# Kernel optimization log

Measured on AMD Instinct MI355X. Metric: run time of the kernel, lower is better.

## Reference

```python
import jax, jax.numpy as jnp
import numpy as np

N_PARTICLES = 100000
STATE_DIM = 64          # 3 + 2*2 + 57
MSG_OUT = 64
HIDDEN = 32
N_EDGES = 1600000


def _init_linear(key, fan_in, fan_out):
    kw, kb = jax.random.split(key)
    bound = 1.0 / np.sqrt(fan_in)
    W = jax.random.uniform(kw, (fan_in, fan_out), minval=-bound, maxval=bound, dtype=jnp.float32)
    b = jax.random.uniform(kb, (fan_out,), minval=-bound, maxval=bound, dtype=jnp.float32)
    return W, b


def setup_inputs() -> dict:
    key = jax.random.key(0)
    ks = jax.random.split(key, 8)
    x = jax.random.normal(ks[0], (N_PARTICLES, STATE_DIM), dtype=jnp.float32)
    edge_index = jax.random.randint(ks[1], (2, N_EDGES), 0, N_PARTICLES, dtype=jnp.int64)
    # message conv MLP: [2*STATE_DIM] -> 32 -> 32 -> MSG_OUT
    mW1, mb1 = _init_linear(ks[2], 2 * STATE_DIM, HIDDEN)
    mW2, mb2 = _init_linear(ks[3], HIDDEN, HIDDEN)
    mW3, mb3 = _init_linear(ks[4], HIDDEN, MSG_OUT)
    # own_state_nn MLP: [STATE_DIM + MSG_OUT] -> 32 -> 32 -> STATE_DIM
    oW1, ob1 = _init_linear(ks[5], STATE_DIM + MSG_OUT, HIDDEN)
    oW2, ob2 = _init_linear(ks[6], HIDDEN, HIDDEN)
    oW3, ob3 = _init_linear(ks[7], HIDDEN, STATE_DIM)
    return {"x": x, "edge_index": edge_index,
            "mW1": mW1, "mb1": mb1, "mW2": mW2, "mb2": mb2, "mW3": mW3, "mb3": mb3,
            "oW1": oW1, "ob1": ob1, "oW2": oW2, "ob2": ob2, "oW3": oW3, "ob3": ob3}


def _mlp3(h, W1, b1, W2, b2, W3, b3):
    h = jax.nn.relu(h @ W1 + b1)
    h = jax.nn.relu(h @ W2 + b2)
    return h @ W3 + b3


def reference(x, edge_index, mW1, mb1, mW2, mb2, mW3, mb3,
              oW1, ob1, oW2, ob2, oW3, ob3):
    src, dst = edge_index[0], edge_index[1]
    # edge-wise message: MLP over [x_src || x_dst]  -> [E, MSG_OUT]
    e_feat = jnp.concatenate([x[src], x[dst]], axis=-1)  # [E, 2*STATE_DIM]
    m = _mlp3(e_feat, mW1, mb1, mW2, mb2, mW3, mb3)
    # scatter-sum aggregation at destination node
    messages = jax.ops.segment_sum(m, dst, num_segments=x.shape[0])  # [N, MSG_OUT]
    combined = jnp.concatenate([x, messages], axis=-1)  # [N, STATE_DIM+MSG_OUT]
    new_state = _mlp3(combined, oW1, ob1, oW2, ob2, oW3, ob3)
    return new_state
```

## Files before the change

### kernel.cpp

```cpp
#include <hip/hip_runtime.h>

#define NP 100000
#define NE 1600000
#define SD 64
#define HID 32
#define MSG 64
#define NP_PAD 100352
#define NTILE (NP / 16)
#define TILE_BLOCKS ((NTILE + 3) / 4)
#define BINSZ 512
#define NBIN ((NP + BINSZ - 1) / BINSZ)
#define EPW 8192
#define NWG ((NE + EPW - 1) / EPW)

typedef float v4f __attribute__((ext_vector_type(4)));
typedef short v4s __attribute__((ext_vector_type(4)));
typedef short v8s __attribute__((ext_vector_type(8)));
typedef __bf16 v8bf __attribute__((ext_vector_type(8)));

#define WQ_FRAGS 56

__device__ __forceinline__ v4f MFMA32(v8s a, v8s b, v4f c) {
  return __builtin_amdgcn_mfma_f32_16x16x32_bf16(
      __builtin_bit_cast(v8bf, a), __builtin_bit_cast(v8bf, b), c, 0, 0, 0);
}

__device__ __forceinline__ short f2bf(float f) {
  return __builtin_bit_cast(short, (__bf16)f);
}
__device__ __forceinline__ float bf2f(short s) {
  unsigned u = ((unsigned)(unsigned short)s) << 16;
  return __builtin_bit_cast(float, u);
}

__device__ __forceinline__ v4f mfma3(v8s ah, v8s al, v8s bh, v8s bl, v4f c) {
  c = MFMA32(al, bh, c);
  c = MFMA32(ah, bl, c);
  c = MFMA32(ah, bh, c);
  return c;
}

__device__ __forceinline__ void load_wfrag(const float* __restrict__ W, int ld,
                                           int kb, int m0, int lq, int l15,
                                           v8s* hi, v8s* lo) {
  v8s h, l;
#pragma unroll
  for (int j = 0; j < 8; ++j) {
    int k = kb + ((j < 4) ? (4 * lq + j) : (16 + 4 * lq + (j - 4)));
    float v = W[k * ld + m0 + l15];
    short hb = f2bf(v);
    h[j] = hb;
    l[j] = f2bf(v - bf2f(hb));
  }
  *hi = h;
  *lo = l;
}

__device__ __forceinline__ void split8(v4f a, v4f b, v8s* hi, v8s* lo) {
  v8s h, l;
#pragma unroll
  for (int j = 0; j < 4; ++j) {
    short ha = f2bf(a[j]); h[j] = ha; l[j] = f2bf(a[j] - bf2f(ha));
    short hb = f2bf(b[j]); h[j + 4] = hb; l[j + 4] = f2bf(b[j] - bf2f(hb));
  }
  *hi = h;
  *lo = l;
}

__device__ __forceinline__ void load_xfrag(const float* xs, int kb, int lq,
                                           v8s* hi, v8s* lo) {
  v4f a = *reinterpret_cast<const v4f*>(xs + kb + 4 * lq);
  v4f b = *reinterpret_cast<const v4f*>(xs + kb + 16 + 4 * lq);
  split8(a, b, hi, lo);
}

__device__ __forceinline__ void chain_frag(v4f d0, v4f d1, v8s* hi, v8s* lo) {
  v4f a, b;
#pragma unroll
  for (int j = 0; j < 4; ++j) {
    a[j] = fmaxf(d0[j], 0.f);
    b[j] = fmaxf(d1[j], 0.f);
  }
  split8(a, b, hi, lo);
}

__device__ __forceinline__ v8s chain_hi(v4f d0, v4f d1) {
  v8s h;
#pragma unroll
  for (int j = 0; j < 4; ++j) {
    h[j] = f2bf(fmaxf(d0[j], 0.f));
    h[j + 4] = f2bf(fmaxf(d1[j], 0.f));
  }
  return h;
}

__global__ __launch_bounds__(256, 2) void setup_kernel(
    const float* __restrict__ x, const int* __restrict__ ei,
    const float* __restrict__ mW1, const float* __restrict__ mb1,
    const float* __restrict__ mW2, const float* __restrict__ mW3,
    const float* __restrict__ oW1, const float* __restrict__ oW2,
    const float* __restrict__ oW3,
    int* __restrict__ gOff, short* __restrict__ wqs,
    float* __restrict__ h1d_buf, short* __restrict__ h1s_buf) {
  __shared__ int cnt[NBIN];
  const int blk = blockIdx.x;

  if (blk < NWG) {
    for (int i = threadIdx.x; i < NBIN; i += 256) cnt[i] = 0;
    __syncthreads();
    const int e0 = blk * EPW;
    const int e1 = (e0 + EPW < NE) ? e0 + EPW : NE;
    for (int e = e0 + threadIdx.x; e < e1; e += 256)
      atomicAdd(&cnt[ei[NE + e] >> 9], 1);
    __syncthreads();
    for (int i = threadIdx.x; i < NBIN; i += 256) gOff[i * NWG + blk] = cnt[i];
    return;
  }

  const int lane = threadIdx.x & 63;
  const int l15 = lane & 15;
  const int lq = lane >> 4;

  if (blk == NWG) {
    if (threadIdx.x >= 64) return;
    v8s* wq = reinterpret_cast<v8s*>(wqs);
    v8s h, l;
#pragma unroll
    for (int t = 0; t < 2; ++t)
#pragma unroll
      for (int kc = 0; kc < 2; ++kc) {
        load_wfrag(mW1, HID, kc * 32, t * 16, lq, l15, &h, &l);
        wq[(t * 2 + kc) * 64 + lane] = h;
        wq[(4 + t * 2 + kc) * 64 + lane] = l;
        load_wfrag(mW1, HID, 64 + kc * 32, t * 16, lq, l15, &h, &l);
        wq[(8 + t * 2 + kc) * 64 + lane] = h;
        wq[(12 + t * 2 + kc) * 64 + lane] = l;
      }
#pragma unroll
    for (int t = 0; t < 2; ++t) {
      load_wfrag(mW2, HID, 0, t * 16, lq, l15, &h, &l);
      wq[(16 + t) * 64 + lane] = h;
      wq[(18 + t) * 64 + lane] = l;
    }
#pragma unroll
    for (int t = 0; t < 4; ++t) {
      load_wfrag(mW3, MSG, 0, t * 16, lq, l15, &h, &l);
      wq[(20 + t) * 64 + lane] = h;
      wq[(24 + t) * 64 + lane] = l;
    }
#pragma unroll
    for (int t = 0; t < 2; ++t)
#pragma unroll
      for (int kc = 0; kc < 4; ++kc) {
        load_wfrag(oW1, HID, kc * 32, t * 16, lq, l15, &h, &l);
        wq[(28 + t * 4 + kc) * 64 + lane] = h;
        wq[(36 + t * 4 + kc) * 64 + lane] = l;
      }
#pragma unroll
    for (int t = 0; t < 2; ++t) {
      load_wfrag(oW2, HID, 0, t * 16, lq, l15, &h, &l);
      wq[(44 + t) * 64 + lane] = h;
      wq[(46 + t) * 64 + lane] = l;
    }
#pragma unroll
    for (int t = 0; t < 4; ++t) {
      load_wfrag(oW3, SD, 0, t * 16, lq, l15, &h, &l);
      wq[(48 + t) * 64 + lane] = h;
      wq[(52 + t) * 64 + lane] = l;
    }
    return;
  }

  const int tile = ((blk - NWG - 1) * 256 + (int)threadIdx.x) >> 6;
  if (tile >= NTILE) return;
  const int node = tile * 16 + l15;

  v4f d0, d1, s0 = {0.f, 0.f, 0.f, 0.f}, s1 = {0.f, 0.f, 0.f, 0.f};
#pragma unroll
  for (int q = 0; q < 4; ++q) {
    d0[q] = mb1[4 * lq + q];
    d1[q] = mb1[16 + 4 * lq + q];
  }
#pragma unroll
  for (int kc = 0; kc < 2; ++kc) {
    v8s xh, xl, wh, wl;
    load_xfrag(x + (size_t)node * SD, kc * 32, lq, &xh, &xl);
    load_wfrag(mW1, HID, 64 + kc * 32, 0, lq, l15, &wh, &wl);
    d0 = mfma3(wh, wl, xh, xl, d0);
    load_wfrag(mW1, HID, 64 + kc * 32, 16, lq, l15, &wh, &wl);
    d1 = mfma3(wh, wl, xh, xl, d1);
    load_wfrag(mW1, HID, kc * 32, 0, lq, l15, &wh, &wl);
    s0 = mfma3(wh, wl, xh, xl, s0);
    load_wfrag(mW1, HID, kc * 32, 16, lq, l15, &wh, &wl);
    s1 = mfma3(wh, wl, xh, xl, s1);
  }
  *reinterpret_cast<v4f*>(h1d_buf + (size_t)node * HID + 4 * lq) = d0;
  *reinterpret_cast<v4f*>(h1d_buf + (size_t)node * HID + 16 + 4 * lq) = d1;
  v4s q0, q1;
#pragma unroll
  for (int q = 0; q < 4; ++q) {
    q0[q] = f2bf(s0[q]);
    q1[q] = f2bf(s1[q]);
  }
  *reinterpret_cast<v4s*>(h1s_buf + (size_t)node * HID + 4 * lq) = q0;
  *reinterpret_cast<v4s*>(h1s_buf + (size_t)node * HID + 16 + 4 * lq) = q1;
}


__global__ __launch_bounds__(256) void scan_bins_kernel(
    int* __restrict__ gOff, int* __restrict__ binStart) {
  __shared__ int sh[256];
  const int b = threadIdx.x;
  int run = 0;
  if (b < NBIN) {
    int4* row = reinterpret_cast<int4*>(gOff + b * NWG);
#pragma unroll 4
    for (int i = 0; i < NWG / 4; ++i) {
      int4 v = row[i];
      int4 w;
      w.x = run; run += v.x;
      w.y = run; run += v.y;
      w.z = run; run += v.z;
      w.w = run; run += v.w;
      row[i] = w;
    }
  }
  sh[b] = run;
  __syncthreads();
  for (int off = 1; off < 256; off <<= 1) {
    int a = (b >= off) ? sh[b - off] : 0;
    __syncthreads();
    sh[b] += a;
    __syncthreads();
  }
  const int excl = sh[b] - run;
  if (b <= NBIN) binStart[b] = excl;
  if (b < NBIN) {
    int4* row = reinterpret_cast<int4*>(gOff + b * NWG);
#pragma unroll 4
    for (int i = 0; i < NWG / 4; ++i) {
      int4 v = row[i];
      v.x += excl; v.y += excl; v.z += excl; v.w += excl;
      row[i] = v;
    }
  }
}

__global__ __launch_bounds__(256) void bin_scatter_kernel(
    const int* __restrict__ ei, const int* __restrict__ gOff,
    unsigned* __restrict__ pairs) {
  __shared__ int cur[NBIN];
  const int w = blockIdx.x;
  for (int i = threadIdx.x; i < NBIN; i += 256) cur[i] = gOff[i * NWG + w];
  __syncthreads();
  const int e0 = w * EPW;
  const int e1 = (e0 + EPW < NE) ? e0 + EPW : NE;
  for (int e = e0 + threadIdx.x; e < e1; e += 256) {
    unsigned s = (unsigned)ei[e];
    unsigned d = (unsigned)ei[NE + e];
    int pos = atomicAdd(&cur[d >> 9], 1);
    pairs[pos] = (s << 9) | (d & (BINSZ - 1));
  }
}

__global__ __launch_bounds__(512) void bin_csr_kernel(
    const unsigned* __restrict__ pairs, const int* __restrict__ binStart,
    int2* __restrict__ co, int* __restrict__ csr_src) {
  __shared__ int sh[BINSZ];
  __shared__ int cu[BINSZ];
  const int b = blockIdx.x;
  const int t = threadIdx.x;
  cu[t] = 0;
  __syncthreads();
  const int p0 = binStart[b], p1 = binStart[b + 1];
  for (int p = p0 + t; p < p1; p += BINSZ)
    atomicAdd(&cu[pairs[p] & (BINSZ - 1)], 1);
  __syncthreads();
  const int v = cu[t];
  sh[t] = v;
  __syncthreads();
  for (int off = 1; off < BINSZ; off <<= 1) {
    int a = (t >= off) ? sh[t - off] : 0;
    __syncthreads();
    sh[t] += a;
    __syncthreads();
  }
  const int excl = sh[t] - v;
  const int node = b * BINSZ + t;
  if (node < NP) co[node] = make_int2(p0 + excl, v);
  cu[t] = excl;
  __syncthreads();
  for (int p = p0 + t; p < p1; p += BINSZ) {
    unsigned pr = pairs[p];
    int loc = atomicAdd(&cu[pr & (BINSZ - 1)], 1);
    csr_src[p0 + loc] = (int)(pr >> 9);
  }
}

__global__ __launch_bounds__(256, 4) void edge_mfma_kernel(
    const short* __restrict__ h1s, const float* __restrict__ h1d_buf,
    const short* __restrict__ wqs, const int2* __restrict__ co,
    const int* __restrict__ csr_src, const float* __restrict__ mb2,
    float* __restrict__ rsum) {
  const int lane = threadIdx.x & 63;
  const int l15 = lane & 15;
  const int lq = lane >> 4;
  const int wid = (blockIdx.x * 256 + threadIdx.x) >> 6;
  const int nw = gridDim.x * 4;
  const v8s* wq = reinterpret_cast<const v8s*>(wqs);

  const v8s w2h0 = wq[16 * 64 + lane], w2h1 = wq[17 * 64 + lane];
  const v8s w2l0 = wq[18 * 64 + lane], w2l1 = wq[19 * 64 + lane];
  v4f bb0, bb1;
#pragma unroll
  for (int q = 0; q < 4; ++q) {
    bb0[q] = mb2[4 * lq + q];
    bb1[q] = mb2[16 + 4 * lq + q];
  }

  for (int n = wid; n < NP; n += nw) {
    const int2 c = co[n];
    const int off = c.x, cnt = c.y;
    const int ng = (cnt + 15) >> 4;

    const v4f h1d0 = *reinterpret_cast<const v4f*>(h1d_buf + (size_t)n * HID + 4 * lq);
    const v4f h1d1 = *reinterpret_cast<const v4f*>(h1d_buf + (size_t)n * HID + 16 + 4 * lq);

    v4f r0 = {0.f, 0.f, 0.f, 0.f}, r1 = {0.f, 0.f, 0.f, 0.f};

    int sa = (l15 < cnt) ? csr_src[off + l15] : 0;
    v4s a0 = *reinterpret_cast<const v4s*>(h1s + (size_t)sa * HID + 4 * lq);
    v4s b0 = *reinterpret_cast<const v4s*>(h1s + (size_t)sa * HID + 16 + 4 * lq);
    int sb = (l15 < cnt - 16) ? csr_src[off + 16 + l15] : 0;
    v4s a1 = *reinterpret_cast<const v4s*>(h1s + (size_t)sb * HID + 4 * lq);
    v4s b1 = *reinterpret_cast<const v4s*>(h1s + (size_t)sb * HID + 16 + 4 * lq);

    int rem = cnt;
    for (int g = 0; g < ng; ++g) {
      int sc = (l15 < rem - 32) ? csr_src[off + (g + 2) * 16 + l15] : 0;

      v4f d0, d1;
#pragma unroll
      for (int q = 0; q < 4; ++q) {
        d0[q] = h1d0[q] + bf2f(a0[q]);
        d1[q] = h1d1[q] + bf2f(b0[q]);
      }

      v8s ph = chain_hi(d0, d1);
      v4f e0 = bb0, e1 = bb1;
      e0 = MFMA32(w2h0, ph, e0);
      e0 = MFMA32(w2l0, ph, e0);
      e1 = MFMA32(w2h1, ph, e1);
      e1 = MFMA32(w2l1, ph, e1);

      if (l15 < rem) {
#pragma unroll
        for (int j = 0; j < 4; ++j) {
          r0[j] += fmaxf(e0[j], 0.f);
          r1[j] += fmaxf(e1[j], 0.f);
        }
      }

      v4s a2 = *reinterpret_cast<const v4s*>(h1s + (size_t)sc * HID + 4 * lq);
      v4s b2 = *reinterpret_cast<const v4s*>(h1s + (size_t)sc * HID + 16 + 4 * lq);

      a0 = a1; b0 = b1;
      a1 = a2; b1 = b2;
      rem -= 16;
    }

#pragma unroll
    for (int j = 0; j < 4; ++j) {
      float a = r0[j], b = r1[j];
      a += __shfl_xor(a, 1); a += __shfl_xor(a, 2);
      a += __shfl_xor(a, 4); a += __shfl_xor(a, 8);
      b += __shfl_xor(b, 1); b += __shfl_xor(b, 2);
      b += __shfl_xor(b, 4); b += __shfl_xor(b, 8);
      r0[j] = a; r1[j] = b;
    }
    if (l15 == 0) {
      *reinterpret_cast<v4f*>(rsum + (size_t)n * HID + 4 * lq) = r0;
      *reinterpret_cast<v4f*>(rsum + (size_t)n * HID + 16 + 4 * lq) = r1;
    }
  }
}

__global__ __launch_bounds__(256, 2) void fused_tail_kernel(
    const float* __restrict__ x, const short* __restrict__ wqs,
    const float* __restrict__ rsum, const int2* __restrict__ co,
    const float* __restrict__ mb3,
    const float* __restrict__ ob1, const float* __restrict__ ob2,
    const float* __restrict__ ob3,
    float* __restrict__ out) {
  const int lane = threadIdx.x & 63;
  const int l15 = lane & 15;
  const int lq = lane >> 4;
  const int tile = (blockIdx.x * 256 + threadIdx.x) >> 6;
  if (tile >= NTILE) return;
  const v8s* wq = reinterpret_cast<const v8s*>(wqs);

  const int node = tile * 16 + l15;
  const float fc = (float)co[node].y;

  v4f ra = *reinterpret_cast<const v4f*>(rsum + (size_t)node * HID + 4 * lq);
  v4f rb = *reinterpret_cast<const v4f*>(rsum + (size_t)node * HID + 16 + 4 * lq);
  v8s bh, bl;
  split8(ra, rb, &bh, &bl);

  v4f m[4];
#pragma unroll
  for (int t = 0; t < 4; ++t) {
    v4f c = {0.f, 0.f, 0.f, 0.f};
    c = mfma3(wq[(20 + t) * 64 + lane], wq[(24 + t) * 64 + lane], bh, bl, c);
#pragma unroll
    for (int q = 0; q < 4; ++q) c[q] += fc * mb3[t * 16 + 4 * lq + q];
    m[t] = c;
  }

  v4f d0, d1;
#pragma unroll
  for (int q = 0; q < 4; ++q) {
    d0[q] = ob1[4 * lq + q];
    d1[q] = ob1[16 + 4 * lq + q];
  }
#pragma unroll
  for (int kc = 0; kc < 2; ++kc) {
    v8s xh, xl;
    load_xfrag(x + (size_t)node * SD, kc * 32, lq, &xh, &xl);
    d0 = mfma3(wq[(28 + kc) * 64 + lane], wq[(36 + kc) * 64 + lane], xh, xl, d0);
    d1 = mfma3(wq[(32 + kc) * 64 + lane], wq[(40 + kc) * 64 + lane], xh, xl, d1);
  }
#pragma unroll
  for (int kc = 0; kc < 2; ++kc) {
    v8s mh, ml;
    split8(m[kc * 2], m[kc * 2 + 1], &mh, &ml);
    d0 = mfma3(wq[(30 + kc) * 64 + lane], wq[(38 + kc) * 64 + lane], mh, ml, d0);
    d1 = mfma3(wq[(34 + kc) * 64 + lane], wq[(42 + kc) * 64 + lane], mh, ml, d1);
  }

  v8s ph, pl;
  chain_frag(d0, d1, &ph, &pl);
  v4f e0, e1;
#pragma unroll
  for (int q = 0; q < 4; ++q) {
    e0[q] = ob2[4 * lq + q];
    e1[q] = ob2[16 + 4 * lq + q];
  }
  e0 = mfma3(wq[44 * 64 + lane], wq[46 * 64 + lane], ph, pl, e0);
  e1 = mfma3(wq[45 * 64 + lane], wq[47 * 64 + lane], ph, pl, e1);

  v8s rh, rl;
  chain_frag(e0, e1, &rh, &rl);
  float* orow = out + (size_t)node * SD;
#pragma unroll
  for (int t = 0; t < 4; ++t) {
    v4f c;
#pragma unroll
    for (int q = 0; q < 4; ++q) c[q] = ob3[t * 16 + 4 * lq + q];
    c = mfma3(wq[(48 + t) * 64 + lane], wq[(52 + t) * 64 + lane], rh, rl, c);
    *reinterpret_cast<v4f*>(orow + t * 16 + 4 * lq) = c;
  }
}

extern "C" void kernel_launch(void* const* d_in, const int* in_sizes, int n_in,
                              void* d_out, int out_size, void* d_ws,
                              size_t ws_size, hipStream_t stream) {
  const float* x = (const float*)d_in[0];
  const int* ei = (const int*)d_in[1];
  const float* mW1 = (const float*)d_in[2];
  const float* mb1 = (const float*)d_in[3];
  const float* mW2 = (const float*)d_in[4];
  const float* mb2 = (const float*)d_in[5];
  const float* mW3 = (const float*)d_in[6];
  const float* mb3 = (const float*)d_in[7];
  const float* oW1 = (const float*)d_in[8];
  const float* ob1 = (const float*)d_in[9];
  const float* oW2 = (const float*)d_in[10];
  const float* ob2 = (const float*)d_in[11];
  const float* oW3 = (const float*)d_in[12];
  const float* ob3 = (const float*)d_in[13];
  float* out = (float*)d_out;

  float* h1d_buf = (float*)d_out;
  short* h1s_buf = (short*)((char*)d_out + (size_t)NP * HID * 4);

  char* p = (char*)d_ws;
  short* wqs = (short*)p;            p += (size_t)WQ_FRAGS * 64 * 16;
  int* gOff = (int*)p;               p += (size_t)NBIN * NWG * 4;
  int* binStart = (int*)p;           p += 200 * 4;
  int2* co = (int2*)p;               p += (size_t)NP_PAD * 8;
  int* csr_src = (int*)p;            p += (size_t)NE * 4;
  unsigned* pairs = (unsigned*)p;
  float* rsum = (float*)p;

  setup_kernel<<<NWG + 1 + TILE_BLOCKS, 256, 0, stream>>>(
      x, ei, mW1, mb1, mW2, mW3, oW1, oW2, oW3, gOff, wqs, h1d_buf, h1s_buf);

  scan_bins_kernel<<<1, 256, 0, stream>>>(gOff, binStart);
  bin_scatter_kernel<<<NWG, 256, 0, stream>>>(ei, gOff, pairs);
  bin_csr_kernel<<<NBIN, 512, 0, stream>>>(pairs, binStart, co, csr_src);

  edge_mfma_kernel<<<2048, 256, 0, stream>>>(
      h1s_buf, h1d_buf, wqs, co, csr_src, mb2, rsum);

  fused_tail_kernel<<<TILE_BLOCKS, 256, 0, stream>>>(
      x, wqs, rsum, co, mb3, ob1, ob2, ob3, out);
}
```

Baseline: 158.8 us.

## Process two destination nodes per wave with interleaved gather pipelines

The per-node edge aggregation kernel now has each wave handle two consecutive destination nodes at once, interleaving their 16-edge groups. The goal is more independent gathers and MFMA chains in flight per wave, hiding gather latency. The prefetch depth per node drops from two groups to one, and the shorter node idles while the longer one finishes, so the wave does divergent, partly wasted iterations. NP is even, so pairing the nodes is safe.

```diff
diff --git a/kernel.cpp b/kernel.cpp
--- a/kernel.cpp
+++ b/kernel.cpp
@@ -318,69 +318,104 @@
     bb1[q] = mb2[16 + 4 * lq + q];
   }
 
-  for (int n = wid; n < NP; n += nw) {
-    const int2 c = co[n];
-    const int off = c.x, cnt = c.y;
-    const int ng = (cnt + 15) >> 4;
-
-    const v4f h1d0 = *reinterpret_cast<const v4f*>(h1d_buf + (size_t)n * HID + 4 * lq);
-    const v4f h1d1 = *reinterpret_cast<const v4f*>(h1d_buf + (size_t)n * HID + 16 + 4 * lq);
-
-    v4f r0 = {0.f, 0.f, 0.f, 0.f}, r1 = {0.f, 0.f, 0.f, 0.f};
-
-    int sa = (l15 < cnt) ? csr_src[off + l15] : 0;
-    v4s a0 = *reinterpret_cast<const v4s*>(h1s + (size_t)sa * HID + 4 * lq);
-    v4s b0 = *reinterpret_cast<const v4s*>(h1s + (size_t)sa * HID + 16 + 4 * lq);
-    int sb = (l15 < cnt - 16) ? csr_src[off + 16 + l15] : 0;
-    v4s a1 = *reinterpret_cast<const v4s*>(h1s + (size_t)sb * HID + 4 * lq);
-    v4s b1 = *reinterpret_cast<const v4s*>(h1s + (size_t)sb * HID + 16 + 4 * lq);
-
-    int rem = cnt;
-    for (int g = 0; g < ng; ++g) {
-      int sc = (l15 < rem - 32) ? csr_src[off + (g + 2) * 16 + l15] : 0;
-
-      v4f d0, d1;
-#pragma unroll
-      for (int q = 0; q < 4; ++q) {
-        d0[q] = h1d0[q] + bf2f(a0[q]);
-        d1[q] = h1d1[q] + bf2f(b0[q]);
-      }
-
-      v8s ph = chain_hi(d0, d1);
-      v4f e0 = bb0, e1 = bb1;
-      e0 = MFMA32(w2h0, ph, e0);
-      e0 = MFMA32(w2l0, ph, e0);
-      e1 = MFMA32(w2h1, ph, e1);
-      e1 = MFMA32(w2l1, ph, e1);
-
-      if (l15 < rem) {
-#pragma unroll
-        for (int j = 0; j < 4; ++j) {
-          r0[j] += fmaxf(e0[j], 0.f);
-          r1[j] += fmaxf(e1[j], 0.f);
+  for (int n = wid * 2; n < NP; n += 2 * nw) {
+    const int4 cc = *reinterpret_cast<const int4*>(co + n);
+    const int offA = cc.x, cntA = cc.y;
+    const int offB = cc.z, cntB = cc.w;
+    const int ngA = (cntA + 15) >> 4;
+    const int ngB = (cntB + 15) >> 4;
+    const int ngM = ngA > ngB ? ngA : ngB;
+
+    const v4f hA0 = *reinterpret_cast<const v4f*>(h1d_buf + (size_t)n * HID + 4 * lq);
+    const v4f hA1 = *reinterpret_cast<const v4f*>(h1d_buf + (size_t)n * HID + 16 + 4 * lq);
+    const v4f hB0 = *reinterpret_cast<const v4f*>(h1d_buf + (size_t)(n + 1) * HID + 4 * lq);
+    const v4f hB1 = *reinterpret_cast<const v4f*>(h1d_buf + (size_t)(n + 1) * HID + 16 + 4 * lq);
+
+    v4f rA0 = {0.f, 0.f, 0.f, 0.f}, rA1 = {0.f, 0.f, 0.f, 0.f};
+    v4f rB0 = {0.f, 0.f, 0.f, 0.f}, rB1 = {0.f, 0.f, 0.f, 0.f};
+
+    int sA = (l15 < cntA) ? csr_src[offA + l15] : 0;
+    int sB = (l15 < cntB) ? csr_src[offB + l15] : 0;
+    v4s aA = *reinterpret_cast<const v4s*>(h1s + (size_t)sA * HID + 4 * lq);
+    v4s bA = *reinterpret_cast<const v4s*>(h1s + (size_t)sA * HID + 16 + 4 * lq);
+    v4s aB = *reinterpret_cast<const v4s*>(h1s + (size_t)sB * HID + 4 * lq);
+    v4s bB = *reinterpret_cast<const v4s*>(h1s + (size_t)sB * HID + 16 + 4 * lq);
+
+    int remA = cntA, remB = cntB;
+    for (int g = 0; g < ngM; ++g) {
+      int sAn = (l15 < remA - 16) ? csr_src[offA + (g + 1) * 16 + l15] : 0;
+      int sBn = (l15 < remB - 16) ? csr_src[offB + (g + 1) * 16 + l15] : 0;
+
+      if (g < ngA) {
+        v4f d0, d1;
+#pragma unroll
+        for (int q = 0; q < 4; ++q) {
+          d0[q] = hA0[q] + bf2f(aA[q]);
+          d1[q] = hA1[q] + bf2f(bA[q]);
+        }
+        v8s ph = chain_hi(d0, d1);
+        v4f e0 = bb0, e1 = bb1;
+        e0 = MFMA32(w2h0, ph, e0);
+        e0 = MFMA32(w2l0, ph, e0);
+        e1 = MFMA32(w2h1, ph, e1);
+        e1 = MFMA32(w2l1, ph, e1);
+        if (l15 < remA) {
+#pragma unroll
+          for (int j = 0; j < 4; ++j) {
+            rA0[j] += fmaxf(e0[j], 0.f);
+            rA1[j] += fmaxf(e1[j], 0.f);
+          }
         }
       }
-
-      v4s a2 = *reinterpret_cast<const v4s*>(h1s + (size_t)sc * HID + 4 * lq);
-      v4s b2 = *reinterpret_cast<const v4s*>(h1s + (size_t)sc * HID + 16 + 4 * lq);
-
-      a0 = a1; b0 = b1;
-      a1 = a2; b1 = b2;
-      rem -= 16;
+      aA = *reinterpret_cast<const v4s*>(h1s + (size_t)sAn * HID + 4 * lq);
+      bA = *reinterpret_cast<const v4s*>(h1s + (size_t)sAn * HID + 16 + 4 * lq);
+
+      if (g < ngB) {
+        v4f d0, d1;
+#pragma unroll
+        for (int q = 0; q < 4; ++q) {
+          d0[q] = hB0[q] + bf2f(aB[q]);
+          d1[q] = hB1[q] + bf2f(bB[q]);
+        }
+        v8s ph = chain_hi(d0, d1);
+        v4f e0 = bb0, e1 = bb1;
+        e0 = MFMA32(w2h0, ph, e0);
+        e0 = MFMA32(w2l0, ph, e0);
+        e1 = MFMA32(w2h1, ph, e1);
+        e1 = MFMA32(w2l1, ph, e1);
+        if (l15 < remB) {
+#pragma unroll
+          for (int j = 0; j < 4; ++j) {
+            rB0[j] += fmaxf(e0[j], 0.f);
+            rB1[j] += fmaxf(e1[j], 0.f);
+          }
+        }
+      }
+      aB = *reinterpret_cast<const v4s*>(h1s + (size_t)sBn * HID + 4 * lq);
+      bB = *reinterpret_cast<const v4s*>(h1s + (size_t)sBn * HID + 16 + 4 * lq);
+
+      remA -= 16;
+      remB -= 16;
     }
 
 #pragma unroll
     for (int j = 0; j < 4; ++j) {
-      float a = r0[j], b = r1[j];
+      float a = rA0[j], b = rA1[j], c = rB0[j], d = rB1[j];
       a += __shfl_xor(a, 1); a += __shfl_xor(a, 2);
       a += __shfl_xor(a, 4); a += __shfl_xor(a, 8);
       b += __shfl_xor(b, 1); b += __shfl_xor(b, 2);
       b += __shfl_xor(b, 4); b += __shfl_xor(b, 8);
-      r0[j] = a; r1[j] = b;
+      c += __shfl_xor(c, 1); c += __shfl_xor(c, 2);
+      c += __shfl_xor(c, 4); c += __shfl_xor(c, 8);
+      d += __shfl_xor(d, 1); d += __shfl_xor(d, 2);
+      d += __shfl_xor(d, 4); d += __shfl_xor(d, 8);
+      rA0[j] = a; rA1[j] = b; rB0[j] = c; rB1[j] = d;
     }
     if (l15 == 0) {
-      *reinterpret_cast<v4f*>(rsum + (size_t)n * HID + 4 * lq) = r0;
-      *reinterpret_cast<v4f*>(rsum + (size_t)n * HID + 16 + 4 * lq) = r1;
+      *reinterpret_cast<v4f*>(rsum + (size_t)n * HID + 4 * lq) = rA0;
+      *reinterpret_cast<v4f*>(rsum + (size_t)n * HID + 16 + 4 * lq) = rA1;
+      *reinterpret_cast<v4f*>(rsum + (size_t)(n + 1) * HID + 4 * lq) = rB0;
+      *reinterpret_cast<v4f*>(rsum + (size_t)(n + 1) * HID + 16 + 4 * lq) = rB1;
     }
   }
 }
```

Result: faster. 154.9 us (median of 3 runs) (-2.4%).

## Drop per-node CSR build; aggregate edge messages per bin with LDS atomics

Applied to the files above, without the earlier changes.

Removes the bin_csr kernel and the per-node CSR walk. A new bin_edge kernel reads the binned (src, local dst) pairs directly, runs the edge MLP with MFMA and accumulates ReLU outputs into a padded LDS tile using float atomics, along with per-node edge counts. Bins shrink to 256 nodes and each bin is split across two blocks that write separate partial sums; the tail kernel adds the two partials. This saves a kernel launch and a full pass over the edge list, but adds many LDS atomics, larger intermediate buffers, and a floating-point summation order that is no longer fixed.

```diff
diff --git a/kernel.cpp b/kernel.cpp
--- a/kernel.cpp
+++ b/kernel.cpp
@@ -8,8 +8,9 @@
 #define NP_PAD 100352
 #define NTILE (NP / 16)
 #define TILE_BLOCKS ((NTILE + 3) / 4)
-#define BINSZ 512
+#define BINSZ 256
 #define NBIN ((NP + BINSZ - 1) / BINSZ)
+#define RPITCH 33
 #define EPW 8192
 #define NWG ((NE + EPW - 1) / EPW)
 
@@ -111,7 +112,7 @@
     const int e0 = blk * EPW;
     const int e1 = (e0 + EPW < NE) ? e0 + EPW : NE;
     for (int e = e0 + threadIdx.x; e < e1; e += 256)
-      atomicAdd(&cnt[ei[NE + e] >> 9], 1);
+      atomicAdd(&cnt[ei[NE + e] >> 8], 1);
     __syncthreads();
     for (int i = threadIdx.x; i < NBIN; i += 256) gOff[i * NWG + blk] = cnt[i];
     return;
@@ -207,9 +208,9 @@
 }
 
 
-__global__ __launch_bounds__(256) void scan_bins_kernel(
+__global__ __launch_bounds__(512) void scan_bins_kernel(
     int* __restrict__ gOff, int* __restrict__ binStart) {
-  __shared__ int sh[256];
+  __shared__ int sh[512];
   const int b = threadIdx.x;
   int run = 0;
   if (b < NBIN) {
@@ -227,7 +228,7 @@
   }
   sh[b] = run;
   __syncthreads();
-  for (int off = 1; off < 256; off <<= 1) {
+  for (int off = 1; off < 512; off <<= 1) {
     int a = (b >= off) ? sh[b - off] : 0;
     __syncthreads();
     sh[b] += a;
@@ -258,57 +259,31 @@
   for (int e = e0 + threadIdx.x; e < e1; e += 256) {
     unsigned s = (unsigned)ei[e];
     unsigned d = (unsigned)ei[NE + e];
-    int pos = atomicAdd(&cur[d >> 9], 1);
-    pairs[pos] = (s << 9) | (d & (BINSZ - 1));
-  }
-}
-
-__global__ __launch_bounds__(512) void bin_csr_kernel(
-    const unsigned* __restrict__ pairs, const int* __restrict__ binStart,
-    int2* __restrict__ co, int* __restrict__ csr_src) {
-  __shared__ int sh[BINSZ];
-  __shared__ int cu[BINSZ];
-  const int b = blockIdx.x;
-  const int t = threadIdx.x;
-  cu[t] = 0;
-  __syncthreads();
-  const int p0 = binStart[b], p1 = binStart[b + 1];
-  for (int p = p0 + t; p < p1; p += BINSZ)
-    atomicAdd(&cu[pairs[p] & (BINSZ - 1)], 1);
-  __syncthreads();
-  const int v = cu[t];
-  sh[t] = v;
-  __syncthreads();
-  for (int off = 1; off < BINSZ; off <<= 1) {
-    int a = (t >= off) ? sh[t - off] : 0;
-    __syncthreads();
-    sh[t] += a;
-    __syncthreads();
-  }
-  const int excl = sh[t] - v;
-  const int node = b * BINSZ + t;
-  if (node < NP) co[node] = make_int2(p0 + excl, v);
-  cu[t] = excl;
-  __syncthreads();
-  for (int p = p0 + t; p < p1; p += BINSZ) {
-    unsigned pr = pairs[p];
-    int loc = atomicAdd(&cu[pr & (BINSZ - 1)], 1);
-    csr_src[p0 + loc] = (int)(pr >> 9);
-  }
-}
-
-__global__ __launch_bounds__(256, 4) void edge_mfma_kernel(
+    int pos = atomicAdd(&cur[d >> 8], 1);
+    pairs[pos] = (s << 8) | (d & (BINSZ - 1));
+  }
+}
+
+__global__ __launch_bounds__(512, 4) void bin_edge_kernel(
     const short* __restrict__ h1s, const float* __restrict__ h1d_buf,
-    const short* __restrict__ wqs, const int2* __restrict__ co,
-    const int* __restrict__ csr_src, const float* __restrict__ mb2,
-    float* __restrict__ rsum) {
-  const int lane = threadIdx.x & 63;
+    const short* __restrict__ wqs, const unsigned* __restrict__ pairs,
+    const int* __restrict__ binStart, const float* __restrict__ mb2,
+    float* __restrict__ rsumP, int* __restrict__ cntP) {
+  __shared__ float r_lds[BINSZ * RPITCH];
+  __shared__ int cnt_lds[BINSZ];
+  const int tid = threadIdx.x;
+  const int lane = tid & 63;
   const int l15 = lane & 15;
   const int lq = lane >> 4;
-  const int wid = (blockIdx.x * 256 + threadIdx.x) >> 6;
-  const int nw = gridDim.x * 4;
+  const int wv = tid >> 6;
+  const int b = blockIdx.x >> 1;
+  const int half = blockIdx.x & 1;
+
+  for (int i = tid; i < BINSZ * RPITCH; i += 512) r_lds[i] = 0.f;
+  for (int i = tid; i < BINSZ; i += 512) cnt_lds[i] = 0;
+  __syncthreads();
+
   const v8s* wq = reinterpret_cast<const v8s*>(wqs);
-
   const v8s w2h0 = wq[16 * 64 + lane], w2h1 = wq[17 * 64 + lane];
   const v8s w2l0 = wq[18 * 64 + lane], w2l1 = wq[19 * 64 + lane];
   v4f bb0, bb1;
@@ -318,76 +293,81 @@
     bb1[q] = mb2[16 + 4 * lq + q];
   }
 
-  for (int n = wid; n < NP; n += nw) {
-    const int2 c = co[n];
-    const int off = c.x, cnt = c.y;
-    const int ng = (cnt + 15) >> 4;
-
-    const v4f h1d0 = *reinterpret_cast<const v4f*>(h1d_buf + (size_t)n * HID + 4 * lq);
-    const v4f h1d1 = *reinterpret_cast<const v4f*>(h1d_buf + (size_t)n * HID + 16 + 4 * lq);
-
-    v4f r0 = {0.f, 0.f, 0.f, 0.f}, r1 = {0.f, 0.f, 0.f, 0.f};
-
-    int sa = (l15 < cnt) ? csr_src[off + l15] : 0;
-    v4s a0 = *reinterpret_cast<const v4s*>(h1s + (size_t)sa * HID + 4 * lq);
-    v4s b0 = *reinterpret_cast<const v4s*>(h1s + (size_t)sa * HID + 16 + 4 * lq);
-    int sb = (l15 < cnt - 16) ? csr_src[off + 16 + l15] : 0;
-    v4s a1 = *reinterpret_cast<const v4s*>(h1s + (size_t)sb * HID + 4 * lq);
-    v4s b1 = *reinterpret_cast<const v4s*>(h1s + (size_t)sb * HID + 16 + 4 * lq);
-
-    int rem = cnt;
-    for (int g = 0; g < ng; ++g) {
-      int sc = (l15 < rem - 32) ? csr_src[off + (g + 2) * 16 + l15] : 0;
-
-      v4f d0, d1;
+  const int p0 = binStart[b], p1 = binStart[b + 1];
+  const int mid = p0 + ((p1 - p0 + 1) >> 1);
+  const int q0 = half ? mid : p0;
+  const int q1 = half ? p1 : mid;
+  const int nodeBase = b * BINSZ;
+
+  int p = q0 + wv * 16;
+  unsigned pr = (p + l15 < q1) ? pairs[p + l15] : 0u;
+  int dl = (int)(pr & (BINSZ - 1));
+  {
+    int src = (int)(pr >> 8);
+  }
+  int src0 = (int)(pr >> 8);
+  v4s a = *reinterpret_cast<const v4s*>(h1s + (size_t)src0 * HID + 4 * lq);
+  v4s c = *reinterpret_cast<const v4s*>(h1s + (size_t)src0 * HID + 16 + 4 * lq);
+  const float* hd = h1d_buf + (size_t)(nodeBase + dl) * HID;
+  v4f hd0 = *reinterpret_cast<const v4f*>(hd + 4 * lq);
+  v4f hd1 = *reinterpret_cast<const v4f*>(hd + 16 + 4 * lq);
+
+  for (; p < q1; p += 128) {
+    const int pn = p + 128 + l15;
+    unsigned prn = (pn < q1) ? pairs[pn] : 0u;
+    int srcn = (int)(prn >> 8);
+    int dln = (int)(prn & (BINSZ - 1));
+    v4s an = *reinterpret_cast<const v4s*>(h1s + (size_t)srcn * HID + 4 * lq);
+    v4s cn = *reinterpret_cast<const v4s*>(h1s + (size_t)srcn * HID + 16 + 4 * lq);
+    const float* hdn = h1d_buf + (size_t)(nodeBase + dln) * HID;
+    v4f hdn0 = *reinterpret_cast<const v4f*>(hdn + 4 * lq);
+    v4f hdn1 = *reinterpret_cast<const v4f*>(hdn + 16 + 4 * lq);
+
+    v4f d0, d1;
+#pragma unroll
+    for (int q = 0; q < 4; ++q) {
+      d0[q] = hd0[q] + bf2f(a[q]);
+      d1[q] = hd1[q] + bf2f(c[q]);
+    }
+    v8s ph = chain_hi(d0, d1);
+    v4f e0 = bb0, e1 = bb1;
+    e0 = MFMA32(w2h0, ph, e0);
+    e0 = MFMA32(w2l0, ph, e0);
+    e1 = MFMA32(w2h1, ph, e1);
+    e1 = MFMA32(w2l1, ph, e1);
+
+    if (p + l15 < q1) {
+      float* rr = r_lds + dl * RPITCH;
 #pragma unroll
       for (int q = 0; q < 4; ++q) {
-        d0[q] = h1d0[q] + bf2f(a0[q]);
-        d1[q] = h1d1[q] + bf2f(b0[q]);
+        atomicAdd(&rr[4 * lq + q], fmaxf(e0[q], 0.f));
+        atomicAdd(&rr[16 + 4 * lq + q], fmaxf(e1[q], 0.f));
       }
-
-      v8s ph = chain_hi(d0, d1);
-      v4f e0 = bb0, e1 = bb1;
-      e0 = MFMA32(w2h0, ph, e0);
-      e0 = MFMA32(w2l0, ph, e0);
-      e1 = MFMA32(w2h1, ph, e1);
-      e1 = MFMA32(w2l1, ph, e1);
-
-      if (l15 < rem) {
-#pragma unroll
-        for (int j = 0; j < 4; ++j) {
-          r0[j] += fmaxf(e0[j], 0.f);
-          r1[j] += fmaxf(e1[j], 0.f);
-        }
-      }
-
-      v4s a2 = *reinterpret_cast<const v4s*>(h1s + (size_t)sc * HID + 4 * lq);
-      v4s b2 = *reinterpret_cast<const v4s*>(h1s + (size_t)sc * HID + 16 + 4 * lq);
-
-      a0 = a1; b0 = b1;
-      a1 = a2; b1 = b2;
-      rem -= 16;
-    }
-
-#pragma unroll
-    for (int j = 0; j < 4; ++j) {
-      float a = r0[j], b = r1[j];
-      a += __shfl_xor(a, 1); a += __shfl_xor(a, 2);
-      a += __shfl_xor(a, 4); a += __shfl_xor(a, 8);
-      b += __shfl_xor(b, 1); b += __shfl_xor(b, 2);
-      b += __shfl_xor(b, 4); b += __shfl_xor(b, 8);
-      r0[j] = a; r1[j] = b;
-    }
-    if (l15 == 0) {
-      *reinterpret_cast<v4f*>(rsum + (size_t)n * HID + 4 * lq) = r0;
-      *reinterpret_cast<v4f*>(rsum + (size_t)n * HID + 16 + 4 * lq) = r1;
-    }
+      if (lq == 0) atomicAdd(&cnt_lds[dl], 1);
+    }
+
+    dl = dln;
+    a = an; c = cn;
+    hd0 = hdn0; hd1 = hdn1;
+  }
+  __syncthreads();
+
+  float* rp = rsumP + (size_t)half * NP_PAD * HID;
+  int* cp = cntP + (size_t)half * NP_PAD;
+  for (int i = tid; i < BINSZ * HID; i += 512) {
+    int nl = i >> 5, row = i & 31;
+    int node = nodeBase + nl;
+    if (node < NP) rp[(size_t)node * HID + row] = r_lds[nl * RPITCH + row];
+  }
+  for (int i = tid; i < BINSZ; i += 512) {
+    int node = nodeBase + i;
+    if (node < NP) cp[node] = cnt_lds[i];
   }
 }
 
 __global__ __launch_bounds__(256, 2) void fused_tail_kernel(
     const float* __restrict__ x, const short* __restrict__ wqs,
-    const float* __restrict__ rsum, const int2* __restrict__ co,
+    const float* __restrict__ rsumP, const int* __restrict__ cntP,
     const float* __restrict__ mb3,
     const float* __restrict__ ob1, const float* __restrict__ ob2,
     const float* __restrict__ ob3,
@@ -400,10 +380,14 @@
   const v8s* wq = reinterpret_cast<const v8s*>(wqs);
 
   const int node = tile * 16 + l15;
-  const float fc = (float)co[node].y;
-
-  v4f ra = *reinterpret_cast<const v4f*>(rsum + (size_t)node * HID + 4 * lq);
-  v4f rb = *reinterpret_cast<const v4f*>(rsum + (size_t)node * HID + 16 + 4 * lq);
+  const float fc = (float)(cntP[node] + cntP[NP_PAD + node]);
+
+  const float* rp0 = rsumP + (size_t)node * HID;
+  const float* rp1 = rsumP + (size_t)NP_PAD * HID + (size_t)node * HID;
+  v4f ra = *reinterpret_cast<const v4f*>(rp0 + 4 * lq) +
+           *reinterpret_cast<const v4f*>(rp1 + 4 * lq);
+  v4f rb = *reinterpret_cast<const v4f*>(rp0 + 16 + 4 * lq) +
+           *reinterpret_cast<const v4f*>(rp1 + 16 + 4 * lq);
   v8s bh, bl;
   split8(ra, rb, &bh, &bl);
 
@@ -487,22 +471,20 @@
   char* p = (char*)d_ws;
   short* wqs = (short*)p;            p += (size_t)WQ_FRAGS * 64 * 16;
   int* gOff = (int*)p;               p += (size_t)NBIN * NWG * 4;
-  int* binStart = (int*)p;           p += 200 * 4;
-  int2* co = (int2*)p;               p += (size_t)NP_PAD * 8;
-  int* csr_src = (int*)p;            p += (size_t)NE * 4;
-  unsigned* pairs = (unsigned*)p;
-  float* rsum = (float*)p;
+  int* binStart = (int*)p;           p += 400 * 4;
+  int* cntP = (int*)p;               p += (size_t)2 * NP_PAD * 4;
+  unsigned* pairs = (unsigned*)p;    p += (size_t)NE * 4;
+  float* rsumP = (float*)p;
 
   setup_kernel<<<NWG + 1 + TILE_BLOCKS, 256, 0, stream>>>(
       x, ei, mW1, mb1, mW2, mW3, oW1, oW2, oW3, gOff, wqs, h1d_buf, h1s_buf);
 
-  scan_bins_kernel<<<1, 256, 0, stream>>>(gOff, binStart);
+  scan_bins_kernel<<<1, 512, 0, stream>>>(gOff, binStart);
   bin_scatter_kernel<<<NWG, 256, 0, stream>>>(ei, gOff, pairs);
-  bin_csr_kernel<<<NBIN, 512, 0, stream>>>(pairs, binStart, co, csr_src);
-
-  edge_mfma_kernel<<<2048, 256, 0, stream>>>(
-      h1s_buf, h1d_buf, wqs, co, csr_src, mb2, rsum);
+
+  bin_edge_kernel<<<NBIN * 2, 512, 0, stream>>>(
+      h1s_buf, h1d_buf, wqs, pairs, binStart, mb2, rsumP, cntP);
 
   fused_tail_kernel<<<TILE_BLOCKS, 256, 0, stream>>>(
-      x, wqs, rsum, co, mb3, ob1, ob2, ob3, out);
-}
+      x, wqs, rsumP, cntP, mb3, ob1, ob2, ob3, out);
+}
```

New measurement: 456.5 us. 2.87x slower.
